# Kernel optimization log

Measured on AMD Instinct MI355X. Metric: run time of the kernel, lower is better.

Reference implementation:

```python
import jax, jax.numpy as jnp
import numpy as np

H = 12  # num_heads

def _alibi_bias(num_heads, n, dtype):
    # slopes: ratio**i for i in 1..H, ratio = 2**(-8/H)
    ratio = 2.0 ** (-8.0 / num_heads)
    slopes = ratio ** jnp.arange(1, num_heads + 1, dtype=jnp.float32)  # [H]
    pos = jnp.arange(n)
    rel = jnp.abs(pos[None, :] - pos[:, None]).astype(jnp.float32)  # [N,N]
    return (-slopes[:, None, None] * rel[None]).astype(dtype)  # [H,N,N]

def setup_inputs() -> dict:
    key = jax.random.key(0)
    ks = jax.random.split(key, 5)
    B, N, C = 16, 1024, 768
    s = 0.02
    return {
        "x": jax.random.normal(ks[0], (B, N, C), jnp.float32),
        "w_qkv": jax.random.normal(ks[1], (3 * C, C), jnp.float32) * s,
        "b_qkv": jax.random.normal(ks[2], (3 * C,), jnp.float32) * s,
        "w_proj": jax.random.normal(ks[3], (C, C), jnp.float32) * s,
        "b_proj": jax.random.normal(ks[4], (C,), jnp.float32) * s,
    }

def reference(x, w_qkv, b_qkv, w_proj, b_proj):
    B, N, C = x.shape
    D = C // H
    scale = D ** -0.5
    qkv = x @ w_qkv.T + b_qkv                       # [B,N,3C]
    qkv = qkv.reshape(B, N, 3, H, D)
    q = qkv[:, :, 0].transpose(0, 2, 1, 3)          # [B,H,N,D]
    k = qkv[:, :, 1].transpose(0, 2, 1, 3)
    v = qkv[:, :, 2].transpose(0, 2, 1, 3)
    bias = _alibi_bias(H, N, x.dtype)               # [H,N,N]
    scores = jnp.einsum('bhnd,bhmd->bhnm', q, k) * scale + bias[None]
    attn = jax.nn.softmax(scores, axis=-1)
    out = jnp.einsum('bhnm,bhmd->bhnd', attn, v)    # [B,H,N,D]
    out = out.transpose(0, 2, 1, 3).reshape(B, N, C)
    return out @ w_proj.T + b_proj
```

## Files before the change

### kernel.cpp

```cpp
#include <hip/hip_runtime.h>


typedef unsigned short u16;
typedef unsigned int u32;
typedef __attribute__((ext_vector_type(8))) short short8;
typedef __attribute__((ext_vector_type(4))) float f32x4;

__device__ __forceinline__ u16 f2bf(float f) {
    u32 u = __float_as_uint(f);
    u32 r = u + 0x7FFFu + ((u >> 16) & 1u);
    return (u16)(r >> 16);
}

__device__ __forceinline__ f32x4 mfma16(short8 a, short8 b, f32x4 c) {
    return __builtin_amdgcn_mfma_f32_16x16x32_bf16(a, b, c, 0, 0, 0);
}
__device__ __forceinline__ u32 cvtpk_bf16(float lo, float hi) {
    u32 r;
    asm("v_cvt_pk_bf16_f32 %0, %1, %2" : "=v"(r) : "v"(lo), "v"(hi));
    return r;
}

typedef __attribute__((address_space(1))) const unsigned int gu32_t;
typedef __attribute__((address_space(3))) unsigned int su32_t;
__device__ __forceinline__ void gl16(const u16* g, u16* s) {
    __builtin_amdgcn_global_load_lds((gu32_t*)g, (su32_t*)s, 16, 0, 0);
}

__global__ void cvt_all(const float* __restrict__ x, const float* __restrict__ wq,
                        const float* __restrict__ wp, u16* __restrict__ Xb,
                        u16* __restrict__ Wqkvb, u16* __restrict__ Wprojb) {
    int i = blockIdx.x * blockDim.x + threadIdx.x;
    int stride = gridDim.x * blockDim.x;
    for (int idx = i; idx < 3735552; idx += stride) {
        const float* src;
        u16* dst;
        int k;
        if (idx < 3145728) { src = x; dst = Xb; k = idx; }
        else if (idx < 3588096) { src = wq; dst = Wqkvb; k = idx - 3145728; }
        else { src = wp; dst = Wprojb; k = idx - 3588096; }
        float4 v = *(const float4*)(src + (size_t)k * 4);
        ushort4 o;
        o.x = f2bf(v.x); o.y = f2bf(v.y); o.z = f2bf(v.z); o.w = f2bf(v.w);
        *(ushort4*)(dst + (size_t)k * 4) = o;
    }
}

template <int EPI>
__global__ __launch_bounds__(512) void gemm_nt(
    const u16* __restrict__ A, const u16* __restrict__ Bw,
    const float* __restrict__ bias, u16* __restrict__ outb, float* __restrict__ outf,
    int nTilesN)
{
    constexpr int K = 768;
    constexpr int nkt = K / 32;
    __shared__ __align__(16) u16 lA[3][128 * 32];
    __shared__ __align__(16) u16 lB[3][128 * 32];

    int tid = threadIdx.x;
    int bid = blockIdx.x;
    int nwg = gridDim.x;
    int cpx = nwg >> 3;
    int swz = (bid & 7) * cpx + (bid >> 3);
    int bm = swz / nTilesN;
    int bn = swz - bm * nTilesN;
    int m0 = bm * 128, n0 = bn * 128;

    int sr = tid >> 2;
    int sc = (tid & 3) << 3;
    const u16* pA = A + (size_t)(m0 + sr) * K + sc;
    const u16* pB = Bw + (size_t)(n0 + sr) * K + sc;
    int lo = tid * 8;

    gl16(pA,      &lA[0][lo]);
    gl16(pB,      &lB[0][lo]);
    gl16(pA + 32, &lA[1][lo]);
    gl16(pB + 32, &lB[1][lo]);

    int w = tid >> 6, lane = tid & 63;
    int wm = w >> 2, wn = w & 3;
    int fq = lane >> 4, fr = lane & 15;
    f32x4 acc[4][2] = {};

    for (int kt = 0; kt < nkt; ++kt) {
        int cur = kt % 3;
        if (kt < nkt - 1) { asm volatile("s_waitcnt vmcnt(2)" ::: "memory"); }
        else              { asm volatile("s_waitcnt vmcnt(0)" ::: "memory"); }
        __builtin_amdgcn_sched_barrier(0);
        __builtin_amdgcn_s_barrier();
        __builtin_amdgcn_sched_barrier(0);
        if (kt + 2 < nkt) {
            int nx = (kt + 2) % 3;
            gl16(pA + (kt + 2) * 32, &lA[nx][lo]);
            gl16(pB + (kt + 2) * 32, &lB[nx][lo]);
        }
        short8 af[4], bfr[2];
#pragma unroll
        for (int i = 0; i < 4; ++i)
            af[i] = *(const short8*)&lA[cur][(wm * 64 + i * 16 + fr) * 32 + fq * 8];
#pragma unroll
        for (int j = 0; j < 2; ++j)
            bfr[j] = *(const short8*)&lB[cur][(wn * 32 + j * 16 + fr) * 32 + fq * 8];
        __builtin_amdgcn_s_setprio(1);
#pragma unroll
        for (int i = 0; i < 4; ++i)
#pragma unroll
            for (int j = 0; j < 2; ++j)
                acc[i][j] = mfma16(af[i], bfr[j], acc[i][j]);
        __builtin_amdgcn_s_setprio(0);
    }

    if (EPI == 0) {
        int b = m0 >> 10;
        int i0 = (m0 & 1023) + wm * 64;
#pragma unroll
        for (int j = 0; j < 2; ++j) {
            int colb = n0 + wn * 32 + j * 16;
            int s = colb / 768;
            int rem = colb % 768;
            int hh = rem >> 6;
            int d0 = rem & 63;
            float bval = bias[colb + fr];
            u16* obase = outb + (((size_t)s * 16 + b) * 12 + hh) * 65536;
#pragma unroll
            for (int i = 0; i < 4; ++i) {
                int r0 = i0 + i * 16 + fq * 4;
#pragma unroll
                for (int r = 0; r < 4; ++r)
                    obase[(size_t)(r0 + r) * 64 + d0 + fr] = f2bf(acc[i][j][r] + bval);
            }
        }
    } else {
#pragma unroll
        for (int j = 0; j < 2; ++j) {
            int col = n0 + wn * 32 + j * 16 + fr;
            float bval = bias[col];
#pragma unroll
            for (int i = 0; i < 4; ++i) {
                int row0 = m0 + wm * 64 + i * 16 + fq * 4;
#pragma unroll
                for (int r = 0; r < 4; ++r)
                    outf[(size_t)(row0 + r) * 768 + col] = acc[i][j][r] + bval;
            }
        }
    }
}

__global__ __launch_bounds__(512) void attn_alibi(
    const u16* __restrict__ QKV, u16* __restrict__ att)
{
    int g = blockIdx.x;
    int xcd = g & 7;
    int idx = g >> 3;
    int qt = idx & 7;
    int bh = xcd * 24 + (idx >> 3);
    int h = bh % 12;
    int b = bh / 12;
    int q0 = qt * 128;
    const u16* Qg = QKV + (size_t)bh * 65536;
    const u16* Kg = QKV + (size_t)(192 + bh) * 65536;
    const u16* Vg = QKV + (size_t)(384 + bh) * 65536;

    __shared__ __align__(16) u16 Ks[64][72];
    __shared__ __align__(16) u16 Vt[64][72];
    __shared__ __align__(16) u16 Ps[128][72];

    int tid = threadIdx.x, w = tid >> 6, lane = tid & 63;
    int fq = lane >> 4, fr = lane & 15;

    short8 aq0 = *(const short8*)(Qg + (size_t)(q0 + w * 16 + fr) * 64 + fq * 8);
    short8 aq1 = *(const short8*)(Qg + (size_t)(q0 + w * 16 + fr) * 64 + 32 + fq * 8);

    const float C1 = 0.125f * 1.44269504f;
    float c2 = __builtin_amdgcn_exp2f(-(2.0f / 3.0f) * (float)(h + 1)) * 1.44269504f;
    int distThr = (int)(40.0f / c2);
    int lo_kv = q0 - 63 - distThr;
    int hi_kv = q0 + 127 + distThr;
    int t_lo = (lo_kv <= 0) ? 0 : (lo_kv >> 6);
    int t_hi = (hi_kv >= 1023) ? 15 : (hi_kv >> 6);

    bool isK = tid < 256;
    int t2 = tid & 255;
    int sr0 = t2 >> 3;
    int sc = (t2 & 7) * 8;
    int vswz = (t2 & 7) << 3;
    int vk0 = sr0 * 2;
    int vcol = vk0 ^ vswz;
    const u16* g0 = isK ? (Kg + (size_t)sr0 * 64 + sc)
                        : (Vg + (size_t)vk0 * 64 + sc);
    const u16* g1 = isK ? (Kg + (size_t)(sr0 + 32) * 64 + sc)
                        : (Vg + (size_t)(vk0 + 1) * 64 + sc);

    uint4 r0 = *(const uint4*)(g0 + (size_t)t_lo * 4096);
    uint4 r1 = *(const uint4*)(g1 + (size_t)t_lo * 4096);

    float di = (float)(q0 + w * 16 + fr - fq * 4);
    float lsum = 0.f;
    f32x4 acc[4] = {};

    for (int it = t_lo; it <= t_hi; ++it) {
        __syncthreads();
        if (isK) {
            *(uint4*)&Ks[sr0][sc] = r0;
            *(uint4*)&Ks[sr0 + 32][sc] = r1;
        } else {
            const u16* v0 = (const u16*)&r0;
            const u16* v1 = (const u16*)&r1;
#pragma unroll
            for (int jj = 0; jj < 8; ++jj)
                *(u32*)&Vt[sc + jj][vcol] = (u32)v0[jj] | ((u32)v1[jj] << 16);
        }
        __syncthreads();

        if (it < t_hi) {
            r0 = *(const uint4*)(g0 + (size_t)(it + 1) * 4096);
            r1 = *(const uint4*)(g1 + (size_t)(it + 1) * 4096);
        }

        f32x4 sfr[4];
        __builtin_amdgcn_s_setprio(1);
#pragma unroll
        for (int ct = 0; ct < 4; ++ct) {
            short8 bk0 = *(const short8*)&Ks[ct * 16 + fr][fq * 8];
            short8 bk1 = *(const short8*)&Ks[ct * 16 + fr][32 + fq * 8];
            f32x4 s0 = {0.f, 0.f, 0.f, 0.f};
            s0 = mfma16(bk0, aq0, s0);
            s0 = mfma16(bk1, aq1, s0);
            sfr[ct] = s0;
        }
        __builtin_amdgcn_s_setprio(0);

        float dkv = di - (float)(it * 64);
#pragma unroll
        for (int ct = 0; ct < 4; ++ct) {
            float t0 = dkv - (float)(ct * 16);
            float e0 = __builtin_amdgcn_exp2f(fmaf(sfr[ct][0], C1, -c2 * fabsf(t0)));
            float e1 = __builtin_amdgcn_exp2f(fmaf(sfr[ct][1], C1, -c2 * fabsf(t0 - 1.0f)));
            float e2 = __builtin_amdgcn_exp2f(fmaf(sfr[ct][2], C1, -c2 * fabsf(t0 - 2.0f)));
            float e3 = __builtin_amdgcn_exp2f(fmaf(sfr[ct][3], C1, -c2 * fabsf(t0 - 3.0f)));
            lsum += (e0 + e1) + (e2 + e3);
            uint2 pk;
            pk.x = cvtpk_bf16(e0, e1);
            pk.y = cvtpk_bf16(e2, e3);
            *(uint2*)&Ps[w * 16 + fr][ct * 16 + fq * 4] = pk;
        }

        short8 pa0 = *(const short8*)&Ps[w * 16 + fr][fq * 8];
        short8 pa1 = *(const short8*)&Ps[w * 16 + fr][32 + fq * 8];
        __builtin_amdgcn_s_setprio(1);
#pragma unroll
        for (int dt = 0; dt < 4; ++dt) {
            int row = dt * 16 + fr;
            int swzr = (row >> 3) << 3;
            short8 bv0 = *(const short8*)&Vt[row][(fq * 8) ^ swzr];
            short8 bv1 = *(const short8*)&Vt[row][(32 + fq * 8) ^ swzr];
            acc[dt] = mfma16(pa0, bv0, acc[dt]);
            acc[dt] = mfma16(pa1, bv1, acc[dt]);
        }
        __builtin_amdgcn_s_setprio(0);
    }

    float l = lsum;
    l += __shfl_xor(l, 16);
    l += __shfl_xor(l, 32);
    float rlo = 1.0f / l;
    float rl[4];
#pragma unroll
    for (int r = 0; r < 4; ++r)
        rl[r] = __shfl(rlo, fq * 4 + r);

#pragma unroll
    for (int dt = 0; dt < 4; ++dt)
#pragma unroll
        for (int r = 0; r < 4; ++r) {
            int ig = q0 + w * 16 + fq * 4 + r;
            att[((size_t)(b * 1024 + ig) * 12 + h) * 64 + dt * 16 + fr] =
                (u16)cvtpk_bf16(acc[dt][r] * rl[r], 0.f);
        }
}

extern "C" void kernel_launch(void* const* d_in, const int* in_sizes, int n_in,
                              void* d_out, int out_size, void* d_ws, size_t ws_size,
                              hipStream_t stream) {
    const float* x      = (const float*)d_in[0];
    const float* w_qkv  = (const float*)d_in[1];
    const float* b_qkv  = (const float*)d_in[2];
    const float* w_proj = (const float*)d_in[3];
    const float* b_proj = (const float*)d_in[4];
    float* out = (float*)d_out;

    char* ws = (char*)d_ws;
    u16* Xb     = (u16*)ws;
    u16* Wqkvb  = (u16*)(ws + 25165824);
    u16* Wprojb = (u16*)(ws + 28704768);
    u16* QKVb   = (u16*)(ws + 29884416);
    u16* Attb   = Xb;

    cvt_all<<<2048, 256, 0, stream>>>(x, w_qkv, w_proj, Xb, Wqkvb, Wprojb);

    gemm_nt<0><<<128 * 18, 512, 0, stream>>>(Xb, Wqkvb, b_qkv, QKVb, nullptr, 18);
    attn_alibi<<<1536, 512, 0, stream>>>(QKVb, Attb);
    gemm_nt<1><<<128 * 6, 512, 0, stream>>>(Attb, Wprojb, b_proj, nullptr, out, 6);
}
```

Before: 190.3 us.

## Enlarge GEMM tiles to 256x256 with BK=64 and split-phase double buffering

Grows the bf16 GEMM block tile from 128x128 to 256x256 with a K-step of 64, so each wave computes a 128x64 sub-tile (8x4 accumulators). The triple-buffered 32-wide pipeline becomes a double-buffered one whose global-to-LDS loads are spread across several barrier-separated MFMA phases within each K-step. The goal is more operand reuse from LDS and fewer barriers per FLOP, with load issue overlapped with compute. In exchange it uses about 128KB of LDS, limits each CU to one block, and launches far fewer blocks (576 for QKV, 192 for proj), which may leave CUs idle on the projection GEMM and adds tail effects.

```diff
diff --git a/kernel.cpp b/kernel.cpp
--- a/kernel.cpp
+++ b/kernel.cpp
@@ -47,15 +47,15 @@
 }
 
 template <int EPI>
-__global__ __launch_bounds__(512) void gemm_nt(
+__global__ __launch_bounds__(512, 1) void gemm_nt(
     const u16* __restrict__ A, const u16* __restrict__ Bw,
     const float* __restrict__ bias, u16* __restrict__ outb, float* __restrict__ outf,
     int nTilesN)
 {
     constexpr int K = 768;
-    constexpr int nkt = K / 32;
-    __shared__ __align__(16) u16 lA[3][128 * 32];
-    __shared__ __align__(16) u16 lB[3][128 * 32];
+    constexpr int nkt = K / 64;
+    __shared__ __align__(16) u16 lA[2][256 * 64];
+    __shared__ __align__(16) u16 lB[2][256 * 64];
 
     int tid = threadIdx.x;
     int bid = blockIdx.x;
@@ -64,58 +64,126 @@
     int swz = (bid & 7) * cpx + (bid >> 3);
     int bm = swz / nTilesN;
     int bn = swz - bm * nTilesN;
-    int m0 = bm * 128, n0 = bn * 128;
-
-    int sr = tid >> 2;
-    int sc = (tid & 3) << 3;
+    int m0 = bm * 256, n0 = bn * 256;
+
+    int sr = tid >> 3;
+    int sc = (tid & 7) << 3;
     const u16* pA = A + (size_t)(m0 + sr) * K + sc;
     const u16* pB = Bw + (size_t)(n0 + sr) * K + sc;
     int lo = tid * 8;
 
-    gl16(pA,      &lA[0][lo]);
-    gl16(pB,      &lB[0][lo]);
-    gl16(pA + 32, &lA[1][lo]);
-    gl16(pB + 32, &lB[1][lo]);
+#define STAGE_A(p, t, e) gl16(pA + (size_t)(e) * 64 * K + (t) * 64, &lA[p][(e) * 4096 + lo])
+#define STAGE_B(p, t, e) gl16(pB + (size_t)(e) * 64 * K + (t) * 64, &lB[p][(e) * 4096 + lo])
+#define ISSUE_B(p, t)   { STAGE_B(p, t, 0); STAGE_B(p, t, 1); STAGE_B(p, t, 2); STAGE_B(p, t, 3); }
+#define ISSUE_AP1(p, t) { STAGE_A(p, t, 0); STAGE_A(p, t, 2); }
+#define ISSUE_AP2(p, t) { STAGE_A(p, t, 1); STAGE_A(p, t, 3); }
+
+    ISSUE_B(0, 0); ISSUE_AP1(0, 0); ISSUE_AP2(0, 0);
+    ISSUE_B(1, 1); ISSUE_AP1(1, 1);
 
     int w = tid >> 6, lane = tid & 63;
     int wm = w >> 2, wn = w & 3;
     int fq = lane >> 4, fr = lane & 15;
-    f32x4 acc[4][2] = {};
-
-    for (int kt = 0; kt < nkt; ++kt) {
-        int cur = kt % 3;
-        if (kt < nkt - 1) { asm volatile("s_waitcnt vmcnt(2)" ::: "memory"); }
-        else              { asm volatile("s_waitcnt vmcnt(0)" ::: "memory"); }
+    f32x4 acc[8][4] = {};
+
+    for (int t = 0; t < nkt; ++t) {
+        int p = t & 1;
+        if (t < nkt - 1) { asm volatile("s_waitcnt vmcnt(6) lgkmcnt(0)" ::: "memory"); }
+        else             { asm volatile("s_waitcnt vmcnt(0) lgkmcnt(0)" ::: "memory"); }
         __builtin_amdgcn_sched_barrier(0);
         __builtin_amdgcn_s_barrier();
         __builtin_amdgcn_sched_barrier(0);
-        if (kt + 2 < nkt) {
-            int nx = (kt + 2) % 3;
-            gl16(pA + (kt + 2) * 32, &lA[nx][lo]);
-            gl16(pB + (kt + 2) * 32, &lB[nx][lo]);
-        }
-        short8 af[4], bfr[2];
-#pragma unroll
-        for (int i = 0; i < 4; ++i)
-            af[i] = *(const short8*)&lA[cur][(wm * 64 + i * 16 + fr) * 32 + fq * 8];
-#pragma unroll
-        for (int j = 0; j < 2; ++j)
-            bfr[j] = *(const short8*)&lB[cur][(wn * 32 + j * 16 + fr) * 32 + fq * 8];
-        __builtin_amdgcn_s_setprio(1);
-#pragma unroll
-        for (int i = 0; i < 4; ++i)
-#pragma unroll
-            for (int j = 0; j < 2; ++j)
-                acc[i][j] = mfma16(af[i], bfr[j], acc[i][j]);
+        if (t + 1 < nkt) ISSUE_AP2(p ^ 1, t + 1);
+
+        short8 bfr[4][2];
+#pragma unroll
+        for (int j = 0; j < 4; ++j)
+#pragma unroll
+            for (int ks = 0; ks < 2; ++ks)
+                bfr[j][ks] = *(const short8*)&lB[p][(wn * 64 + j * 16 + fr) * 64 + ks * 32 + fq * 8];
+        short8 af[2][2];
+#pragma unroll
+        for (int di = 0; di < 2; ++di)
+#pragma unroll
+            for (int ks = 0; ks < 2; ++ks)
+                af[di][ks] = *(const short8*)&lA[p][(wm * 128 + (0 + di) * 16 + fr) * 64 + ks * 32 + fq * 8];
+        __builtin_amdgcn_s_setprio(1);
+#pragma unroll
+        for (int di = 0; di < 2; ++di)
+#pragma unroll
+            for (int j = 0; j < 4; ++j) {
+                acc[di][j] = mfma16(af[di][0], bfr[j][0], acc[di][j]);
+                acc[di][j] = mfma16(af[di][1], bfr[j][1], acc[di][j]);
+            }
+        __builtin_amdgcn_s_setprio(0);
+        asm volatile("s_waitcnt lgkmcnt(0)" ::: "memory");
+        __builtin_amdgcn_sched_barrier(0);
+        __builtin_amdgcn_s_barrier();
+        __builtin_amdgcn_sched_barrier(0);
+
+        if (t + 2 < nkt) ISSUE_B(p, t + 2);
+#pragma unroll
+        for (int di = 0; di < 2; ++di)
+#pragma unroll
+            for (int ks = 0; ks < 2; ++ks)
+                af[di][ks] = *(const short8*)&lA[p][(wm * 128 + (2 + di) * 16 + fr) * 64 + ks * 32 + fq * 8];
+        __builtin_amdgcn_s_setprio(1);
+#pragma unroll
+        for (int di = 0; di < 2; ++di)
+#pragma unroll
+            for (int j = 0; j < 4; ++j) {
+                acc[2 + di][j] = mfma16(af[di][0], bfr[j][0], acc[2 + di][j]);
+                acc[2 + di][j] = mfma16(af[di][1], bfr[j][1], acc[2 + di][j]);
+            }
+        __builtin_amdgcn_s_setprio(0);
+        asm volatile("s_waitcnt lgkmcnt(0)" ::: "memory");
+        __builtin_amdgcn_sched_barrier(0);
+        __builtin_amdgcn_s_barrier();
+        __builtin_amdgcn_sched_barrier(0);
+
+        if (t + 2 < nkt) ISSUE_AP1(p, t + 2);
+#pragma unroll
+        for (int di = 0; di < 2; ++di)
+#pragma unroll
+            for (int ks = 0; ks < 2; ++ks)
+                af[di][ks] = *(const short8*)&lA[p][(wm * 128 + (4 + di) * 16 + fr) * 64 + ks * 32 + fq * 8];
+        __builtin_amdgcn_s_setprio(1);
+#pragma unroll
+        for (int di = 0; di < 2; ++di)
+#pragma unroll
+            for (int j = 0; j < 4; ++j) {
+                acc[4 + di][j] = mfma16(af[di][0], bfr[j][0], acc[4 + di][j]);
+                acc[4 + di][j] = mfma16(af[di][1], bfr[j][1], acc[4 + di][j]);
+            }
+        __builtin_amdgcn_s_setprio(0);
+
+#pragma unroll
+        for (int di = 0; di < 2; ++di)
+#pragma unroll
+            for (int ks = 0; ks < 2; ++ks)
+                af[di][ks] = *(const short8*)&lA[p][(wm * 128 + (6 + di) * 16 + fr) * 64 + ks * 32 + fq * 8];
+        __builtin_amdgcn_s_setprio(1);
+#pragma unroll
+        for (int di = 0; di < 2; ++di)
+#pragma unroll
+            for (int j = 0; j < 4; ++j) {
+                acc[6 + di][j] = mfma16(af[di][0], bfr[j][0], acc[6 + di][j]);
+                acc[6 + di][j] = mfma16(af[di][1], bfr[j][1], acc[6 + di][j]);
+            }
         __builtin_amdgcn_s_setprio(0);
     }
+#undef STAGE_A
+#undef STAGE_B
+#undef ISSUE_B
+#undef ISSUE_AP1
+#undef ISSUE_AP2
 
     if (EPI == 0) {
         int b = m0 >> 10;
-        int i0 = (m0 & 1023) + wm * 64;
-#pragma unroll
-        for (int j = 0; j < 2; ++j) {
-            int colb = n0 + wn * 32 + j * 16;
+        int i0 = (m0 & 1023) + wm * 128;
+#pragma unroll
+        for (int j = 0; j < 4; ++j) {
+            int colb = n0 + wn * 64 + j * 16;
             int s = colb / 768;
             int rem = colb % 768;
             int hh = rem >> 6;
@@ -123,7 +191,7 @@
             float bval = bias[colb + fr];
             u16* obase = outb + (((size_t)s * 16 + b) * 12 + hh) * 65536;
 #pragma unroll
-            for (int i = 0; i < 4; ++i) {
+            for (int i = 0; i < 8; ++i) {
                 int r0 = i0 + i * 16 + fq * 4;
 #pragma unroll
                 for (int r = 0; r < 4; ++r)
@@ -132,12 +200,12 @@
         }
     } else {
 #pragma unroll
-        for (int j = 0; j < 2; ++j) {
-            int col = n0 + wn * 32 + j * 16 + fr;
+        for (int j = 0; j < 4; ++j) {
+            int col = n0 + wn * 64 + j * 16 + fr;
             float bval = bias[col];
 #pragma unroll
-            for (int i = 0; i < 4; ++i) {
-                int row0 = m0 + wm * 64 + i * 16 + fq * 4;
+            for (int i = 0; i < 8; ++i) {
+                int row0 = m0 + wm * 128 + i * 16 + fq * 4;
 #pragma unroll
                 for (int r = 0; r < 4; ++r)
                     outf[(size_t)(row0 + r) * 768 + col] = acc[i][j][r] + bval;
@@ -298,7 +366,7 @@
 
     cvt_all<<<2048, 256, 0, stream>>>(x, w_qkv, w_proj, Xb, Wqkvb, Wprojb);
 
-    gemm_nt<0><<<128 * 18, 512, 0, stream>>>(Xb, Wqkvb, b_qkv, QKVb, nullptr, 18);
+    gemm_nt<0><<<64 * 9, 512, 0, stream>>>(Xb, Wqkvb, b_qkv, QKVb, nullptr, 9);
     attn_alibi<<<1536, 512, 0, stream>>>(QKVb, Attb);
-    gemm_nt<1><<<128 * 6, 512, 0, stream>>>(Attb, Wprojb, b_proj, nullptr, out, 6);
-}
+    gemm_nt<1><<<64 * 3, 512, 0, stream>>>(Attb, Wprojb, b_proj, nullptr, out, 3);
+}
```

Result: slower. 258.9 us (+36.1%).

## Load K fragments directly from global memory and tighten ALiBi tile window

Applied to the files above, without the earlier changes.

Removes the LDS staging buffer for K so each wave reads its K MFMA operands directly from global memory, leaving only V transposed through shared memory by half the threads. The ALiBi distance threshold for skipping far KV tiles is lowered, so fewer tiles are processed per query block. This cuts LDS traffic and the tile loop count, but adds un-prefetched global load latency on the critical MFMA path and redundant K reads across waves. The tighter cutoff also drops slightly larger softmax contributions.

```diff
diff --git a/kernel.cpp b/kernel.cpp
--- a/kernel.cpp
+++ b/kernel.cpp
@@ -161,7 +161,6 @@
     const u16* Kg = QKV + (size_t)(192 + bh) * 65536;
     const u16* Vg = QKV + (size_t)(384 + bh) * 65536;
 
-    __shared__ __align__(16) u16 Ks[64][72];
     __shared__ __align__(16) u16 Vt[64][72];
     __shared__ __align__(16) u16 Ps[128][72];
 
@@ -173,37 +172,35 @@
 
     const float C1 = 0.125f * 1.44269504f;
     float c2 = __builtin_amdgcn_exp2f(-(2.0f / 3.0f) * (float)(h + 1)) * 1.44269504f;
-    int distThr = (int)(40.0f / c2);
+    int distThr = (int)(32.0f / c2);
     int lo_kv = q0 - 63 - distThr;
     int hi_kv = q0 + 127 + distThr;
     int t_lo = (lo_kv <= 0) ? 0 : (lo_kv >> 6);
     int t_hi = (hi_kv >= 1023) ? 15 : (hi_kv >> 6);
 
-    bool isK = tid < 256;
+    bool isV = tid >= 256;
     int t2 = tid & 255;
-    int sr0 = t2 >> 3;
     int sc = (t2 & 7) * 8;
     int vswz = (t2 & 7) << 3;
-    int vk0 = sr0 * 2;
+    int vk0 = (t2 >> 3) * 2;
     int vcol = vk0 ^ vswz;
-    const u16* g0 = isK ? (Kg + (size_t)sr0 * 64 + sc)
-                        : (Vg + (size_t)vk0 * 64 + sc);
-    const u16* g1 = isK ? (Kg + (size_t)(sr0 + 32) * 64 + sc)
-                        : (Vg + (size_t)(vk0 + 1) * 64 + sc);
-
-    uint4 r0 = *(const uint4*)(g0 + (size_t)t_lo * 4096);
-    uint4 r1 = *(const uint4*)(g1 + (size_t)t_lo * 4096);
+    const u16* g0 = Vg + (size_t)vk0 * 64 + sc;
+    const u16* g1 = Vg + (size_t)(vk0 + 1) * 64 + sc;
+
+    uint4 r0, r1;
+    if (isV) {
+        r0 = *(const uint4*)(g0 + (size_t)t_lo * 4096);
+        r1 = *(const uint4*)(g1 + (size_t)t_lo * 4096);
+    }
 
     float di = (float)(q0 + w * 16 + fr - fq * 4);
     float lsum = 0.f;
     f32x4 acc[4] = {};
 
     for (int it = t_lo; it <= t_hi; ++it) {
+        int kv0 = it * 64;
         __syncthreads();
-        if (isK) {
-            *(uint4*)&Ks[sr0][sc] = r0;
-            *(uint4*)&Ks[sr0 + 32][sc] = r1;
-        } else {
+        if (isV) {
             const u16* v0 = (const u16*)&r0;
             const u16* v1 = (const u16*)&r1;
 #pragma unroll
@@ -212,7 +209,7 @@
         }
         __syncthreads();
 
-        if (it < t_hi) {
+        if (isV && it < t_hi) {
             r0 = *(const uint4*)(g0 + (size_t)(it + 1) * 4096);
             r1 = *(const uint4*)(g1 + (size_t)(it + 1) * 4096);
         }
@@ -221,8 +218,9 @@
         __builtin_amdgcn_s_setprio(1);
 #pragma unroll
         for (int ct = 0; ct < 4; ++ct) {
-            short8 bk0 = *(const short8*)&Ks[ct * 16 + fr][fq * 8];
-            short8 bk1 = *(const short8*)&Ks[ct * 16 + fr][32 + fq * 8];
+            const u16* krow = Kg + (size_t)(kv0 + ct * 16 + fr) * 64;
+            short8 bk0 = *(const short8*)(krow + fq * 8);
+            short8 bk1 = *(const short8*)(krow + 32 + fq * 8);
             f32x4 s0 = {0.f, 0.f, 0.f, 0.f};
             s0 = mfma16(bk0, aq0, s0);
             s0 = mfma16(bk1, aq1, s0);
@@ -230,7 +228,7 @@
         }
         __builtin_amdgcn_s_setprio(0);
 
-        float dkv = di - (float)(it * 64);
+        float dkv = di - (float)kv0;
 #pragma unroll
         for (int ct = 0; ct < 4; ++ct) {
             float t0 = dkv - (float)(ct * 16);
```

Measured after the change: 275.8 us. 44.9% more time.
